# Kernel optimization log

Measured on AMD Instinct MI355X. Metric: run time of the kernel, lower is better.

## Reference

```python
import jax, jax.numpy as jnp
import numpy as np

NUM_HEADS = 16


def setup_inputs() -> dict:
    key = jax.random.key(0)
    k1, k2, k3 = jax.random.split(key, 3)
    B, L, H = 2, 2048, 1024
    return {
        "key": jax.random.normal(k1, (B, L, H), dtype=jnp.float32),
        "W_ctx": jax.random.normal(k2, (H, H), dtype=jnp.float32) * (1.0 / np.sqrt(H)),
        "b_ctx": jax.random.normal(k3, (H,), dtype=jnp.float32) * 0.01,
    }


def reference(key, W_ctx, b_ctx):
    # Note: the torch module defines q/k/v Linear layers but never calls them
    # in forward(); it reshapes the raw input into heads directly.
    B, L, H = key.shape
    dh = H // NUM_HEADS
    # [B, L, H] -> [B, nh, L, dh]
    x = key.reshape(B, L, NUM_HEADS, dh).transpose(0, 2, 1, 3)
    # QK^T then scale by sqrt(head_dim) (key.shape[-1] after head split)
    scores = jnp.einsum("bhqd,bhkd->bhqk", x, x) * (1.0 / np.float32(np.sqrt(dh)))
    attn = jax.nn.softmax(scores, axis=-1)  # dropout p treated as eval/identity
    ctx = jnp.einsum("bhqk,bhkd->bhqd", attn, x)
    # [B, nh, L, dh] -> [B, L, H]
    ctx = ctx.transpose(0, 2, 1, 3).reshape(B, L, H)
    # context_transform: nn.Linear(H, H, bias=True)
    return ctx @ W_ctx.T + b_ctx
```

## Files before the change

kernel.cpp:

```cpp
#include <hip/hip_runtime.h>
#include <stdint.h>

#define NH     16
#define LSEQ   2048
#define DH     64
#define HDIM   1024
#define BATCH  2

typedef __attribute__((ext_vector_type(8))) short bf16x8;
typedef __attribute__((ext_vector_type(8))) unsigned short u16x8;
typedef __attribute__((ext_vector_type(4))) float f32x4;
typedef __attribute__((ext_vector_type(16))) float f32x16;

static __device__ inline unsigned short f2bs(float f) {
    union { float f; uint32_t u; } v; v.f = f;
    uint32_t u = v.u;
    return (unsigned short)((u + 0x7FFFu + ((u >> 16) & 1u)) >> 16);
}

static __device__ inline unsigned int cvtpk(float lo, float hi) {
    unsigned int r;
    asm("v_cvt_pk_bf16_f32 %0, %1, %2" : "=v"(r) : "v"(lo), "v"(hi));
    return r;
}
static __device__ inline void pl32swap(unsigned int &a, unsigned int &b) {
    asm volatile("v_permlane32_swap_b32 %0, %1" : "+v"(a), "+v"(b));
}

#define GLOAD_LDS(gp, lp) \
    __builtin_amdgcn_global_load_lds((const __attribute__((address_space(1))) void*)(gp), \
                                     (__attribute__((address_space(3))) void*)(lp), 16, 0, 0)

#define MFMA32(A, B, C) __builtin_amdgcn_mfma_f32_32x32x16_bf16((A), (B), (C), 0, 0, 0)

#define QK_SCALE 0.42466083f

__global__ __launch_bounds__(256) void prep_kernel(const float* __restrict__ x,
                                                   const float* __restrict__ W,
                                                   unsigned short* __restrict__ xb,
                                                   unsigned short* __restrict__ xt,
                                                   unsigned short* __restrict__ wbt) {
    const int lt = blockIdx.x, bh = blockIdx.y;
    const int bid = bh * 32 + lt;
    const int t = threadIdx.x;

    if (t < 128) {
        const int gid = bid * 128 + t;
        const int n  = gid >> 7;
        const int kc = gid & 127;
        const float* src = W + (size_t)n * 1024 + kc * 8;
        float4 f0 = *(const float4*)(src);
        float4 f1 = *(const float4*)(src + 4);
        u16x8 v;
        v[0]=f2bs(f0.x); v[1]=f2bs(f0.y); v[2]=f2bs(f0.z); v[3]=f2bs(f0.w);
        v[4]=f2bs(f1.x); v[5]=f2bs(f1.y); v[6]=f2bs(f1.z); v[7]=f2bs(f1.w);
        const int nt = n >> 7, rn = n & 127;
        const int kt = kc >> 3, c = kc & 7;
        *(u16x8*)(wbt + (((size_t)nt * 16 + kt) * 128 + rn) * 64 + ((c ^ (rn & 7)) * 8)) = v;
    }

    const int b = bh >> 4, h = bh & 15;
    const int r = t >> 2, cp = t & 3;

    __shared__ __align__(16) unsigned short Sm[64][72];

    const float* src = x + ((size_t)(b * LSEQ + lt * 64 + r)) * HDIM + h * DH + cp * 16;
    float4 f0 = *(const float4*)(src);
    float4 f1 = *(const float4*)(src + 4);
    float4 f2 = *(const float4*)(src + 8);
    float4 f3 = *(const float4*)(src + 12);
    u16x8 lo, hi;
    lo[0]=f2bs(f0.x); lo[1]=f2bs(f0.y); lo[2]=f2bs(f0.z); lo[3]=f2bs(f0.w);
    lo[4]=f2bs(f1.x); lo[5]=f2bs(f1.y); lo[6]=f2bs(f1.z); lo[7]=f2bs(f1.w);
    hi[0]=f2bs(f2.x); hi[1]=f2bs(f2.y); hi[2]=f2bs(f2.z); hi[3]=f2bs(f2.w);
    hi[4]=f2bs(f3.x); hi[5]=f2bs(f3.y); hi[6]=f2bs(f3.z); hi[7]=f2bs(f3.w);
    u16x8 slo, shi;
    slo[0]=f2bs(f0.x*QK_SCALE); slo[1]=f2bs(f0.y*QK_SCALE); slo[2]=f2bs(f0.z*QK_SCALE); slo[3]=f2bs(f0.w*QK_SCALE);
    slo[4]=f2bs(f1.x*QK_SCALE); slo[5]=f2bs(f1.y*QK_SCALE); slo[6]=f2bs(f1.z*QK_SCALE); slo[7]=f2bs(f1.w*QK_SCALE);
    shi[0]=f2bs(f2.x*QK_SCALE); shi[1]=f2bs(f2.y*QK_SCALE); shi[2]=f2bs(f2.z*QK_SCALE); shi[3]=f2bs(f2.w*QK_SCALE);
    shi[4]=f2bs(f3.x*QK_SCALE); shi[5]=f2bs(f3.y*QK_SCALE); shi[6]=f2bs(f3.z*QK_SCALE); shi[7]=f2bs(f3.w*QK_SCALE);

    {
        unsigned short* xbase = xb + (size_t)bh * 131072
                              + ((size_t)lt * 2 + (r >> 5)) * 2048 + cp * 512 + (r & 31) * 8;
        *(u16x8*)(xbase)       = slo;
        *(u16x8*)(xbase + 256) = shi;
    }
    *(u16x8*)&Sm[r][cp * 16]     = lo;
    *(u16x8*)&Sm[r][cp * 16 + 8] = hi;
    __syncthreads();

    {
        const int d = t >> 2, part = (t & 3) * 16;
        unsigned short* vbase = xt + (size_t)bh * 131072 + (size_t)lt * 4096
                              + (d >> 5) * 2048 + (part >> 4) * 512 + (d & 31) * 8;
        u16x8 g0, g1;
        #pragma unroll
        for (int i = 0; i < 8; ++i) g0[i] = Sm[part + i][d];
        #pragma unroll
        for (int i = 0; i < 8; ++i) g1[i] = Sm[part + 8 + i][d];
        *(u16x8*)(vbase)       = g0;
        *(u16x8*)(vbase + 256) = g1;
    }
}

__global__ __launch_bounds__(256, 3) void attn_kernel(const unsigned short* __restrict__ xb,
                                                      const unsigned short* __restrict__ xt,
                                                      unsigned short* __restrict__ ctxt) {
    const int bh = blockIdx.x;
    const int qt = blockIdx.y;
    const int tid = threadIdx.x;
    const int w = tid >> 6, lane = tid & 63;
    const int l31 = lane & 31, hh = lane >> 5;

    const char* xbB = (const char*)(xb + (size_t)bh * 131072);
    const char* xtB = (const char*)(xt + (size_t)bh * 131072);

    bf16x8 qf[4];
    {
        const char* qbase = xbB + (size_t)(qt * 4 + w) * 4096 + lane * 16;
        #pragma unroll
        for (int ds = 0; ds < 4; ++ds)
            qf[ds] = *(const bf16x8*)(qbase + ds * 1024);
    }

    bf16x8 ones;
    #pragma unroll
    for (int i = 0; i < 8; ++i) ones[i] = (short)0x3F80;

    f32x16 accA, accB, accS;
    #pragma unroll
    for (int r = 0; r < 16; ++r) { accA[r] = 0.f; accB[r] = 0.f; accS[r] = 0.f; }

    const char* ka = xbB + lane * 16;
    const char* va = xtB + lane * 16;

    for (int tt = 0; tt < 32; ++tt) {
        bf16x8 kfa[4], kfb[4];
        #pragma unroll
        for (int ds = 0; ds < 4; ++ds) {
            kfa[ds] = *(const bf16x8*)(ka + ds * 1024);
            kfb[ds] = *(const bf16x8*)(ka + 4096 + ds * 1024);
        }

        f32x16 s0, s1;
        #pragma unroll
        for (int r = 0; r < 16; ++r) { s0[r] = 0.f; s1[r] = 0.f; }
        __builtin_amdgcn_s_setprio(1);
        #pragma unroll
        for (int ds = 0; ds < 4; ++ds) {
            s0 = MFMA32(kfa[ds], qf[ds], s0);
            s1 = MFMA32(kfb[ds], qf[ds], s1);
        }
        __builtin_amdgcn_s_setprio(0);

        bf16x8 vfa[4], vfb[4];
        #pragma unroll
        for (int ks = 0; ks < 4; ++ks) {
            vfa[ks] = *(const bf16x8*)(va + ks * 1024);
            vfb[ks] = *(const bf16x8*)(va + 4096 + ks * 1024);
        }
        ka += 8192;
        va += 8192;

        #pragma unroll
        for (int r = 0; r < 16; ++r) {
            s0[r] = __builtin_amdgcn_exp2f(s0[r]);
            s1[r] = __builtin_amdgcn_exp2f(s1[r]);
        }

        bf16x8 pa[4];
        #pragma unroll
        for (int ks = 0; ks < 4; ++ks) {
            const int r0 = (ks & 1) * 8;
            unsigned int x0, y0, x1, y1;
            if (ks < 2) {
                x0 = cvtpk(s0[r0 + 0], s0[r0 + 1]);
                y0 = cvtpk(s0[r0 + 4], s0[r0 + 5]);
                x1 = cvtpk(s0[r0 + 2], s0[r0 + 3]);
                y1 = cvtpk(s0[r0 + 6], s0[r0 + 7]);
            } else {
                x0 = cvtpk(s1[r0 + 0], s1[r0 + 1]);
                y0 = cvtpk(s1[r0 + 4], s1[r0 + 5]);
                x1 = cvtpk(s1[r0 + 2], s1[r0 + 3]);
                y1 = cvtpk(s1[r0 + 6], s1[r0 + 7]);
            }
            pl32swap(x0, y0);
            pl32swap(x1, y1);
            union { unsigned int u[4]; bf16x8 v; } pu;
            pu.u[0] = x0; pu.u[1] = x1; pu.u[2] = y0; pu.u[3] = y1;
            pa[ks] = pu.v;
        }

        __builtin_amdgcn_s_setprio(1);
        #pragma unroll
        for (int ks = 0; ks < 4; ++ks) {
            accA = MFMA32(pa[ks], vfa[ks], accA);
            accB = MFMA32(pa[ks], vfb[ks], accB);
            accS = MFMA32(pa[ks], ones, accS);
        }
        __builtin_amdgcn_s_setprio(0);
    }

    const int b = bh >> 4, hd = bh & 15;
    const int mt = b * 16 + qt;
    unsigned short* tbase = ctxt + ((size_t)mt * 16 + hd) * 128 * 64;
    const int c80 = l31 >> 3, c81 = 4 + (l31 >> 3), ce = l31 & 7;
    #pragma unroll
    for (int r = 0; r < 16; ++r) {
        const float iv = 1.0f / accS[r];
        const int crow = (r & 3) + 8 * (r >> 2) + 4 * hh;
        const int rr = w * 32 + crow;
        unsigned short* rowp = tbase + rr * 64;
        const int sw = rr & 7;
        rowp[((c80 ^ sw) * 8) + ce] = f2bs(accA[r] * iv);
        rowp[((c81 ^ sw) * 8) + ce] = f2bs(accB[r] * iv);
    }
}

__global__ __launch_bounds__(256) void proj_kernel(const unsigned short* __restrict__ ctxt,
                                                   const unsigned short* __restrict__ wbt,
                                                   const float* __restrict__ bias,
                                                   float* __restrict__ out) {
    const int ntb = blockIdx.x;
    const int mtb = blockIdx.y;
    const int tid = threadIdx.x;
    const int w = tid >> 6, lane = tid & 63;
    const int la = lane & 15, quad = lane >> 4;
    const int wm = (w >> 1) * 64, wn = (w & 1) * 64;

    __shared__ __align__(16) unsigned short As[2][8192];
    __shared__ __align__(16) unsigned short Bs[2][8192];

    const unsigned short* abase = ctxt + (size_t)mtb * 16 * 8192;
    const unsigned short* bbase = wbt  + (size_t)ntb * 16 * 8192;

    const int sw0 = ((quad)     ^ (la & 7)) * 8;
    const int sw1 = ((quad + 4) ^ (la & 7)) * 8;

    const f32x4 fzero = {0.f, 0.f, 0.f, 0.f};
    f32x4 acc[4][4];
    #pragma unroll
    for (int i = 0; i < 4; ++i)
        #pragma unroll
        for (int j = 0; j < 4; ++j) acc[i][j] = fzero;

    #pragma unroll
    for (int j = 0; j < 4; ++j) {
        const int fc = j * 256 + tid;
        GLOAD_LDS((const char*)abase + fc * 16, (char*)As[0] + fc * 16);
        GLOAD_LDS((const char*)bbase + fc * 16, (char*)Bs[0] + fc * 16);
    }
    __syncthreads();

    for (int kt = 0; kt < 16; ++kt) {
        if (kt < 15) {
            const char* asrc = (const char*)(abase + (kt + 1) * 8192);
            const char* bsrc = (const char*)(bbase + (kt + 1) * 8192);
            char* adst = (char*)As[(kt + 1) & 1];
            char* bdst = (char*)Bs[(kt + 1) & 1];
            #pragma unroll
            for (int j = 0; j < 4; ++j) {
                const int fc = j * 256 + tid;
                GLOAD_LDS(asrc + fc * 16, adst + fc * 16);
                GLOAD_LDS(bsrc + fc * 16, bdst + fc * 16);
            }
        }

        const unsigned short* Ab = As[kt & 1];
        const unsigned short* Bb = Bs[kt & 1];
        #pragma unroll
        for (int ks2 = 0; ks2 < 2; ++ks2) {
            const int sw = ks2 ? sw1 : sw0;
            bf16x8 af[4], bfr[4];
            #pragma unroll
            for (int mt = 0; mt < 4; ++mt) af[mt]  = *(const bf16x8*)&Ab[(wm + mt * 16 + la) * 64 + sw];
            #pragma unroll
            for (int nt = 0; nt < 4; ++nt) bfr[nt] = *(const bf16x8*)&Bb[(wn + nt * 16 + la) * 64 + sw];
            #pragma unroll
            for (int mt = 0; mt < 4; ++mt)
                #pragma unroll
                for (int nt = 0; nt < 4; ++nt)
                    acc[mt][nt] = __builtin_amdgcn_mfma_f32_16x16x32_bf16(af[mt], bfr[nt], acc[mt][nt], 0, 0, 0);
        }
        __syncthreads();
    }

    const int m0 = mtb * 128, n0 = ntb * 128;
    #pragma unroll
    for (int nt = 0; nt < 4; ++nt) {
        const int n = n0 + wn + nt * 16 + la;
        const float bv = bias[n];
        #pragma unroll
        for (int mt = 0; mt < 4; ++mt)
            #pragma unroll
            for (int r = 0; r < 4; ++r) {
                const int m = m0 + wm + mt * 16 + quad * 4 + r;
                out[(size_t)m * HDIM + n] = acc[mt][nt][r] + bv;
            }
    }
}

extern "C" void kernel_launch(void* const* d_in, const int* in_sizes, int n_in,
                              void* d_out, int out_size, void* d_ws, size_t ws_size,
                              hipStream_t stream) {
    const float* x    = (const float*)d_in[0];
    const float* W    = (const float*)d_in[1];
    const float* bias = (const float*)d_in[2];
    float* out = (float*)d_out;

    unsigned short* ctxt = (unsigned short*)d_ws;
    unsigned short* xbp  = (unsigned short*)((char*)d_ws + ( 8u << 20));
    unsigned short* xtp  = (unsigned short*)((char*)d_ws + (16u << 20));
    unsigned short* wbt  = (unsigned short*)((char*)d_ws + (24u << 20));

    prep_kernel<<<dim3(32, 32), 256, 0, stream>>>(x, W, xbp, xtp, wbt);
    attn_kernel<<<dim3(32, 16), 256, 0, stream>>>(xbp, xtp, ctxt);
    proj_kernel<<<dim3(8, 32), 256, 0, stream>>>(ctxt, wbt, bias, out);
}
```

Measured before the change: 142.8 us.

## Split attention key range across two wave groups and combine via LDS

Each attention block now runs 512 threads. Two groups of four waves each process half of the key sequence for the same query tile. The second group writes its partial numerator and denominator accumulators to shared memory, and the first group adds them in before normalizing and storing. This doubles the active waves per block so more latency can be hidden and each wave's serial loop is halved, at the cost of 48KB of LDS per block, a barrier, and a reduction step that may limit occupancy.

```diff
diff --git a/kernel.cpp b/kernel.cpp
--- a/kernel.cpp
+++ b/kernel.cpp
@@ -104,21 +104,26 @@
     }
 }
 
-__global__ __launch_bounds__(256, 3) void attn_kernel(const unsigned short* __restrict__ xb,
+__global__ __launch_bounds__(512, 4) void attn_kernel(const unsigned short* __restrict__ xb,
                                                       const unsigned short* __restrict__ xt,
                                                       unsigned short* __restrict__ ctxt) {
     const int bh = blockIdx.x;
     const int qt = blockIdx.y;
     const int tid = threadIdx.x;
-    const int w = tid >> 6, lane = tid & 63;
+    const int w = tid >> 6;
+    const int half = w >> 2;
+    const int wq = w & 3;
+    const int lane = tid & 63;
     const int l31 = lane & 31, hh = lane >> 5;
+
+    __shared__ __align__(16) float cmb[12288];
 
     const char* xbB = (const char*)(xb + (size_t)bh * 131072);
     const char* xtB = (const char*)(xt + (size_t)bh * 131072);
 
     bf16x8 qf[4];
     {
-        const char* qbase = xbB + (size_t)(qt * 4 + w) * 4096 + lane * 16;
+        const char* qbase = xbB + (size_t)(qt * 4 + wq) * 4096 + lane * 16;
         #pragma unroll
         for (int ds = 0; ds < 4; ++ds)
             qf[ds] = *(const bf16x8*)(qbase + ds * 1024);
@@ -132,10 +137,10 @@
     #pragma unroll
     for (int r = 0; r < 16; ++r) { accA[r] = 0.f; accB[r] = 0.f; accS[r] = 0.f; }
 
-    const char* ka = xbB + lane * 16;
-    const char* va = xtB + lane * 16;
-
-    for (int tt = 0; tt < 32; ++tt) {
+    const char* ka = xbB + (size_t)half * 16 * 8192 + lane * 16;
+    const char* va = xtB + (size_t)half * 16 * 8192 + lane * 16;
+
+    for (int it = 0; it < 16; ++it) {
         bf16x8 kfa[4], kfb[4];
         #pragma unroll
         for (int ds = 0; ds < 4; ++ds) {
@@ -202,19 +207,48 @@
         __builtin_amdgcn_s_setprio(0);
     }
 
-    const int b = bh >> 4, hd = bh & 15;
-    const int mt = b * 16 + qt;
-    unsigned short* tbase = ctxt + ((size_t)mt * 16 + hd) * 128 * 64;
-    const int c80 = l31 >> 3, c81 = 4 + (l31 >> 3), ce = l31 & 7;
-    #pragma unroll
-    for (int r = 0; r < 16; ++r) {
-        const float iv = 1.0f / accS[r];
-        const int crow = (r & 3) + 8 * (r >> 2) + 4 * hh;
-        const int rr = w * 32 + crow;
-        unsigned short* rowp = tbase + rr * 64;
-        const int sw = rr & 7;
-        rowp[((c80 ^ sw) * 8) + ce] = f2bs(accA[r] * iv);
-        rowp[((c81 ^ sw) * 8) + ce] = f2bs(accB[r] * iv);
+    if (half) {
+        float* b = cmb + (size_t)wq * 3072 + lane * 4;
+        #pragma unroll
+        for (int g = 0; g < 4; ++g) {
+            f32x4 cA = { accA[g*4+0], accA[g*4+1], accA[g*4+2], accA[g*4+3] };
+            f32x4 cB = { accB[g*4+0], accB[g*4+1], accB[g*4+2], accB[g*4+3] };
+            f32x4 cS = { accS[g*4+0], accS[g*4+1], accS[g*4+2], accS[g*4+3] };
+            *(f32x4*)(b +    0 + g * 256) = cA;
+            *(f32x4*)(b + 1024 + g * 256) = cB;
+            *(f32x4*)(b + 2048 + g * 256) = cS;
+        }
+    }
+    __syncthreads();
+    if (!half) {
+        const float* b = cmb + (size_t)wq * 3072 + lane * 4;
+        #pragma unroll
+        for (int g = 0; g < 4; ++g) {
+            f32x4 cA = *(const f32x4*)(b +    0 + g * 256);
+            f32x4 cB = *(const f32x4*)(b + 1024 + g * 256);
+            f32x4 cS = *(const f32x4*)(b + 2048 + g * 256);
+            #pragma unroll
+            for (int j = 0; j < 4; ++j) {
+                accA[g*4+j] += cA[j];
+                accB[g*4+j] += cB[j];
+                accS[g*4+j] += cS[j];
+            }
+        }
+
+        const int bb = bh >> 4, hd = bh & 15;
+        const int mt = bb * 16 + qt;
+        unsigned short* tbase = ctxt + ((size_t)mt * 16 + hd) * 128 * 64;
+        const int c80 = l31 >> 3, c81 = 4 + (l31 >> 3), ce = l31 & 7;
+        #pragma unroll
+        for (int r = 0; r < 16; ++r) {
+            const float iv = 1.0f / accS[r];
+            const int crow = (r & 3) + 8 * (r >> 2) + 4 * hh;
+            const int rr = wq * 32 + crow;
+            unsigned short* rowp = tbase + rr * 64;
+            const int sw = rr & 7;
+            rowp[((c80 ^ sw) * 8) + ce] = f2bs(accA[r] * iv);
+            rowp[((c81 ^ sw) * 8) + ce] = f2bs(accB[r] * iv);
+        }
     }
 }
 
@@ -315,6 +349,6 @@
     unsigned short* wbt  = (unsigned short*)((char*)d_ws + (24u << 20));
 
     prep_kernel<<<dim3(32, 32), 256, 0, stream>>>(x, W, xbp, xtp, wbt);
-    attn_kernel<<<dim3(32, 16), 256, 0, stream>>>(xbp, xtp, ctxt);
+    attn_kernel<<<dim3(32, 16), 512, 0, stream>>>(xbp, xtp, ctxt);
     proj_kernel<<<dim3(8, 32), 256, 0, stream>>>(ctxt, wbt, bias, out);
 }
```

Result: slower. 189.5 us (+32.7%).

## Split attention head dim across wave pairs to double grid parallelism

Applied to the files above, without the earlier changes.

Each workgroup now covers two 32-row query groups instead of four, and each pair of waves splits the 64-wide value dimension into two halves. The grid doubles to 1024 blocks and each wave holds one output accumulator instead of two. This should raise occupancy and spread work over more CUs. The cost is that QK^T scores and exp2 are computed twice per query group, once per d-half wave, so matrix-core and exp work per output rises.

```diff
diff --git a/kernel.cpp b/kernel.cpp
--- a/kernel.cpp
+++ b/kernel.cpp
@@ -108,17 +108,21 @@
                                                       const unsigned short* __restrict__ xt,
                                                       unsigned short* __restrict__ ctxt) {
     const int bh = blockIdx.x;
-    const int qt = blockIdx.y;
+    const int qp = blockIdx.y;
     const int tid = threadIdx.x;
-    const int w = tid >> 6, lane = tid & 63;
+    const int w = tid >> 6;
+    const int wql = w & 1;
+    const int dh = w >> 1;
+    const int lane = tid & 63;
     const int l31 = lane & 31, hh = lane >> 5;
+    const int gs = qp * 2 + wql;
 
     const char* xbB = (const char*)(xb + (size_t)bh * 131072);
     const char* xtB = (const char*)(xt + (size_t)bh * 131072);
 
     bf16x8 qf[4];
     {
-        const char* qbase = xbB + (size_t)(qt * 4 + w) * 4096 + lane * 16;
+        const char* qbase = xbB + (size_t)gs * 4096 + lane * 16;
         #pragma unroll
         for (int ds = 0; ds < 4; ++ds)
             qf[ds] = *(const bf16x8*)(qbase + ds * 1024);
@@ -128,12 +132,12 @@
     #pragma unroll
     for (int i = 0; i < 8; ++i) ones[i] = (short)0x3F80;
 
-    f32x16 accA, accB, accS;
-    #pragma unroll
-    for (int r = 0; r < 16; ++r) { accA[r] = 0.f; accB[r] = 0.f; accS[r] = 0.f; }
+    f32x16 acc, accS;
+    #pragma unroll
+    for (int r = 0; r < 16; ++r) { acc[r] = 0.f; accS[r] = 0.f; }
 
     const char* ka = xbB + lane * 16;
-    const char* va = xtB + lane * 16;
+    const char* va = xtB + dh * 4096 + lane * 16;
 
     for (int tt = 0; tt < 32; ++tt) {
         bf16x8 kfa[4], kfb[4];
@@ -154,12 +158,10 @@
         }
         __builtin_amdgcn_s_setprio(0);
 
-        bf16x8 vfa[4], vfb[4];
-        #pragma unroll
-        for (int ks = 0; ks < 4; ++ks) {
-            vfa[ks] = *(const bf16x8*)(va + ks * 1024);
-            vfb[ks] = *(const bf16x8*)(va + 4096 + ks * 1024);
-        }
+        bf16x8 vf[4];
+        #pragma unroll
+        for (int ks = 0; ks < 4; ++ks)
+            vf[ks] = *(const bf16x8*)(va + ks * 1024);
         ka += 8192;
         va += 8192;
 
@@ -195,26 +197,24 @@
         __builtin_amdgcn_s_setprio(1);
         #pragma unroll
         for (int ks = 0; ks < 4; ++ks) {
-            accA = MFMA32(pa[ks], vfa[ks], accA);
-            accB = MFMA32(pa[ks], vfb[ks], accB);
+            acc  = MFMA32(pa[ks], vf[ks], acc);
             accS = MFMA32(pa[ks], ones, accS);
         }
         __builtin_amdgcn_s_setprio(0);
     }
 
     const int b = bh >> 4, hd = bh & 15;
-    const int mt = b * 16 + qt;
+    const int mt = b * 16 + (gs >> 2);
     unsigned short* tbase = ctxt + ((size_t)mt * 16 + hd) * 128 * 64;
-    const int c80 = l31 >> 3, c81 = 4 + (l31 >> 3), ce = l31 & 7;
+    const int c8 = dh * 4 + (l31 >> 3), ce = l31 & 7;
     #pragma unroll
     for (int r = 0; r < 16; ++r) {
         const float iv = 1.0f / accS[r];
         const int crow = (r & 3) + 8 * (r >> 2) + 4 * hh;
-        const int rr = w * 32 + crow;
+        const int rr = (gs & 3) * 32 + crow;
         unsigned short* rowp = tbase + rr * 64;
         const int sw = rr & 7;
-        rowp[((c80 ^ sw) * 8) + ce] = f2bs(accA[r] * iv);
-        rowp[((c81 ^ sw) * 8) + ce] = f2bs(accB[r] * iv);
+        rowp[((c8 ^ sw) * 8) + ce] = f2bs(acc[r] * iv);
     }
 }
 
@@ -315,6 +315,6 @@
     unsigned short* wbt  = (unsigned short*)((char*)d_ws + (24u << 20));
 
     prep_kernel<<<dim3(32, 32), 256, 0, stream>>>(x, W, xbp, xtp, wbt);
-    attn_kernel<<<dim3(32, 16), 256, 0, stream>>>(xbp, xtp, ctxt);
+    attn_kernel<<<dim3(32, 32), 256, 0, stream>>>(xbp, xtp, ctxt);
     proj_kernel<<<dim3(8, 32), 256, 0, stream>>>(ctxt, wbt, bias, out);
 }
```

New measurement: 169.4 us. +18.6%, slower.

## Triple-buffer projection GEMM LDS tiles with two-stage-ahead prefetch

Applied to the files above, without the earlier changes.

The output projection GEMM moves from double to triple buffering in LDS, so global-to-LDS loads are issued two k-tiles ahead. Full syncthreads waits are replaced by partial vmcnt waits plus a raw barrier, so one stage's loads can stay in flight during compute. This doubles the LDS footprint to 96KB per block, which may reduce occupancy. Correctness relies on the vmcnt counts matching the eight loads issued per stage.

```diff
diff --git a/kernel.cpp b/kernel.cpp
--- a/kernel.cpp
+++ b/kernel.cpp
@@ -229,8 +229,8 @@
     const int la = lane & 15, quad = lane >> 4;
     const int wm = (w >> 1) * 64, wn = (w & 1) * 64;
 
-    __shared__ __align__(16) unsigned short As[2][8192];
-    __shared__ __align__(16) unsigned short Bs[2][8192];
+    __shared__ __align__(16) unsigned short As[3][8192];
+    __shared__ __align__(16) unsigned short Bs[3][8192];
 
     const unsigned short* abase = ctxt + (size_t)mtb * 16 * 8192;
     const unsigned short* bbase = wbt  + (size_t)ntb * 16 * 8192;
@@ -246,29 +246,34 @@
         for (int j = 0; j < 4; ++j) acc[i][j] = fzero;
 
     #pragma unroll
-    for (int j = 0; j < 4; ++j) {
-        const int fc = j * 256 + tid;
-        GLOAD_LDS((const char*)abase + fc * 16, (char*)As[0] + fc * 16);
-        GLOAD_LDS((const char*)bbase + fc * 16, (char*)Bs[0] + fc * 16);
-    }
-    __syncthreads();
+    for (int s = 0; s < 2; ++s) {
+        const char* asrc = (const char*)(abase + s * 8192);
+        const char* bsrc = (const char*)(bbase + s * 8192);
+        #pragma unroll
+        for (int j = 0; j < 4; ++j) {
+            const int fc = j * 256 + tid;
+            GLOAD_LDS(asrc + fc * 16, (char*)As[s] + fc * 16);
+            GLOAD_LDS(bsrc + fc * 16, (char*)Bs[s] + fc * 16);
+        }
+    }
+    asm volatile("s_waitcnt vmcnt(8)" ::: "memory");
+    __builtin_amdgcn_s_barrier();
 
     for (int kt = 0; kt < 16; ++kt) {
-        if (kt < 15) {
-            const char* asrc = (const char*)(abase + (kt + 1) * 8192);
-            const char* bsrc = (const char*)(bbase + (kt + 1) * 8192);
-            char* adst = (char*)As[(kt + 1) & 1];
-            char* bdst = (char*)Bs[(kt + 1) & 1];
+        if (kt < 14) {
+            const int nb = (kt + 2) % 3;
+            const char* asrc = (const char*)(abase + (kt + 2) * 8192);
+            const char* bsrc = (const char*)(bbase + (kt + 2) * 8192);
             #pragma unroll
             for (int j = 0; j < 4; ++j) {
                 const int fc = j * 256 + tid;
-                GLOAD_LDS(asrc + fc * 16, adst + fc * 16);
-                GLOAD_LDS(bsrc + fc * 16, bdst + fc * 16);
+                GLOAD_LDS(asrc + fc * 16, (char*)As[nb] + fc * 16);
+                GLOAD_LDS(bsrc + fc * 16, (char*)Bs[nb] + fc * 16);
             }
         }
 
-        const unsigned short* Ab = As[kt & 1];
-        const unsigned short* Bb = Bs[kt & 1];
+        const unsigned short* Ab = As[kt % 3];
+        const unsigned short* Bb = Bs[kt % 3];
         #pragma unroll
         for (int ks2 = 0; ks2 < 2; ++ks2) {
             const int sw = ks2 ? sw1 : sw0;
@@ -283,7 +288,14 @@
                 for (int nt = 0; nt < 4; ++nt)
                     acc[mt][nt] = __builtin_amdgcn_mfma_f32_16x16x32_bf16(af[mt], bfr[nt], acc[mt][nt], 0, 0, 0);
         }
-        __syncthreads();
+
+        if (kt < 14) {
+            asm volatile("s_waitcnt vmcnt(8)" ::: "memory");
+            __builtin_amdgcn_s_barrier();
+        } else if (kt == 14) {
+            asm volatile("s_waitcnt vmcnt(0)" ::: "memory");
+            __builtin_amdgcn_s_barrier();
+        }
     }
 
     const int m0 = mtb * 128, n0 = ntb * 128;
```

Measured after the change: 142.6 us. Within noise of the previous version (-0.1%).
